# Kernel tuning notes

Measured on AMD Instinct MI355X. Metric: run time of the kernel, lower is better.

Reference implementation:

```python
import jax, jax.numpy as jnp
import numpy as np

ALPHA = 0.99   # config.alpha_grape
GAMMA = 0.999  # config.gamma
LAMBD = 0.7    # config.lambd_grape
T, A = 262144, 64


def setup_inputs() -> dict:
    key = jax.random.key(0)
    ks = jax.random.split(key, 7)
    q = jax.random.normal(ks[0], (T + 1, A), jnp.float32)
    q_tar = jax.random.normal(ks[1], (T + 1, A), jnp.float32)
    # pi / mu are probability distributions over actions (softmax of logits)
    pi = jax.nn.softmax(jax.random.normal(ks[2], (T + 1, A), jnp.float32), axis=-1)
    mu_t = jax.nn.softmax(jax.random.normal(ks[3], (T, A), jnp.float32), axis=-1)
    a_t = jax.random.randint(ks[4], (T,), 0, A, dtype=jnp.int32)
    r_t = jax.random.normal(ks[5], (T,), jnp.float32)
    done_t = jax.random.randint(ks[6], (T,), 0, 2, dtype=jnp.int32)
    return dict(q=q, q_tar=q_tar, pi=pi, a_t=a_t, r_t=r_t, mu_t=mu_t, done_t=done_t)


def reference(q, q_tar, pi, a_t, r_t, mu_t, done_t):
    # GRAPE.compute_targets
    l = q.shape[0] - 1
    idx = jnp.arange(l)
    pi_t, pi_tp1 = pi[:-1], pi[1:]
    q_t, q_tp1 = q[:-1], q_tar[1:]
    q_t_a = q_t[idx, a_t]                              # [T]
    v_t = jnp.sum(pi_t * q_t, axis=1)                  # [T]
    v_tp1 = jnp.sum(pi_tp1 * q_tp1, axis=1)            # [T]
    done_f = done_t.astype(q.dtype)
    q_t_a_est = r_t + (1.0 - done_f) * GAMMA * v_tp1
    td_error = q_t_a_est - q_t_a
    rho_t_a = pi_t[idx, a_t] / mu_t[idx, a_t]
    c_t_a = LAMBD * jnp.clip(rho_t_a, 0.0, 1.0)

    # backward-in-time first-order recurrence over y'
    def step(y_prime, xs):
        est, td, rho, c, d = xs
        y = jnp.where(d > 0.5, 0.0, y_prime)           # reset at episode end
        g = est + y
        y_new = LAMBD * GAMMA * rho * td + GAMMA * c * y
        return y_new, g

    _, g_q = jax.lax.scan(
        step, jnp.float32(0.0),
        (q_t_a_est, td_error, rho_t_a, c_t_a, done_f),
        reverse=True,
    )
    targets_q = g_q + ALPHA * (q_t_a - v_t)            # [T]
    advantages = (1.0 - ALPHA) * (q_t - v_t[:, None])  # [T, A]
    return targets_q, advantages
```

## Files before the change

### kernel.cpp

```cpp
#include <hip/hip_runtime.h>

#define GAMMA 0.999f
#define LAMBD 0.7f
#define ALPHA 0.99f

constexpr int A_DIM = 64;
constexpr int CH    = 256;
constexpr int BLK   = 256;

typedef float fx4 __attribute__((ext_vector_type(4)));

__device__ __forceinline__ float dot4(const float4& a, const float4& b) {
    return a.x*b.x + a.y*b.y + a.z*b.z + a.w*b.w;
}
__device__ __forceinline__ void nt_store4(float* p, float x, float y, float z, float w) {
    fx4 v = { x, y, z, w };
    __builtin_nontemporal_store(v, (fx4*)p);
}

__global__ __launch_bounds__(BLK, 4)
void k_main(const float* __restrict__ q, const float* __restrict__ q_tar,
            const float* __restrict__ pi, const int* __restrict__ a_t,
            const float* __restrict__ r_t, const float* __restrict__ mu_t,
            const int* __restrict__ done_t,
            float* __restrict__ adv_out, float* __restrict__ targets,
            float2* __restrict__ combL, float2* __restrict__ cab)
{
    __shared__ float sQa[CH], sPa[CH], sMa[CH], sKm[CH], sRt[CH];
    __shared__ float sV[CH], sVp[CH + 1];
    __shared__ float sCA[4], sCB[4];

    const int tid  = threadIdx.x;
    const int wave = tid >> 6, lane = tid & 63;
    const int sub  = lane >> 4, li = lane & 15;
    const int R0   = blockIdx.x * CH;

    {
        int r = R0 + tid;
        int a = a_t[r];
        sQa[tid] = q[r * A_DIM + a];
        sPa[tid] = pi[r * A_DIM + a];
        sMa[tid] = mu_t[r * A_DIM + a];
        sRt[tid] = r_t[r];
        sKm[tid] = 1.0f - (float)done_t[r];
    }
    if (tid >= 192 && tid < 208) {
        int l16 = tid - 192;
        int gE  = (R0 + CH) * A_DIM + l16 * 4;
        float4 pe = *(const float4*)&pi[gE];
        float4 qe = *(const float4*)&q_tar[gE];
        float d = dot4(pe, qe);
        #pragma unroll
        for (int off = 1; off < 16; off <<= 1) d += __shfl_xor(d, off);
        if (l16 == 0) sVp[CH] = d;
    }

    const int lrow0 = wave * 64 + sub;
    float4 piA, qA, qtA, piB, qB, qtB;
    {
        int gA = (R0 + lrow0) * A_DIM + li * 4;
        int gB = gA + 4 * A_DIM;
        piA = *(const float4*)&pi[gA];
        qA  = *(const float4*)&q[gA];
        qtA = *(const float4*)&q_tar[gA];
        piB = *(const float4*)&pi[gB];
        qB  = *(const float4*)&q[gB];
        qtB = *(const float4*)&q_tar[gB];
    }
    #pragma unroll
    for (int i = 0; i < 8; ++i) {
        float4 npiA, nqA, nqtA, npiB, nqB, nqtB;
        if (i < 7) {
            int gA = (R0 + lrow0 + (i + 1) * 8) * A_DIM + li * 4;
            int gB = gA + 4 * A_DIM;
            npiA = *(const float4*)&pi[gA];
            nqA  = *(const float4*)&q[gA];
            nqtA = *(const float4*)&q_tar[gA];
            npiB = *(const float4*)&pi[gB];
            nqB  = *(const float4*)&q[gB];
            nqtB = *(const float4*)&q_tar[gB];
        }

        int lrowA = lrow0 + i * 8;
        int lrowB = lrowA + 4;
        int gA = (R0 + lrowA) * A_DIM + li * 4;
        int gB = (R0 + lrowB) * A_DIM + li * 4;

        float d1A = dot4(piA, qA),  d2A = dot4(piA, qtA);
        float d1B = dot4(piB, qB),  d2B = dot4(piB, qtB);
        #pragma unroll
        for (int off = 1; off < 16; off <<= 1) {
            d1A += __shfl_xor(d1A, off);
            d2A += __shfl_xor(d2A, off);
            d1B += __shfl_xor(d1B, off);
            d2B += __shfl_xor(d2B, off);
        }

        nt_store4(&adv_out[gA],
                  (1.0f - ALPHA) * (qA.x - d1A), (1.0f - ALPHA) * (qA.y - d1A),
                  (1.0f - ALPHA) * (qA.z - d1A), (1.0f - ALPHA) * (qA.w - d1A));
        nt_store4(&adv_out[gB],
                  (1.0f - ALPHA) * (qB.x - d1B), (1.0f - ALPHA) * (qB.y - d1B),
                  (1.0f - ALPHA) * (qB.z - d1B), (1.0f - ALPHA) * (qB.w - d1B));

        if (li == 0) {
            sV[lrowA] = d1A;  sVp[lrowA] = d2A;
            sV[lrowB] = d1B;  sVp[lrowB] = d2B;
        }

        piA = npiA; qA = nqA; qtA = nqtA;
        piB = npiB; qB = nqB; qtB = nqtB;
    }
    __syncthreads();

    const int row = tid;
    float s0 = sV[row];
    float s1 = sVp[row + 1];
    float kmask = sKm[row];
    float qa  = sQa[row];
    float rho = sPa[row] / sMa[row];
    float est = sRt[row] + kmask * (GAMMA * s1);
    float td  = est - qa;
    float c   = LAMBD * fminf(fmaxf(rho, 0.0f), 1.0f);
    float Fa  = (LAMBD * GAMMA) * rho * td;
    float Fb  = kmask * (GAMMA * c);
    float E   = est + ALPHA * (qa - s0);

    float Ai = Fa, Bi = Fb;
    #pragma unroll
    for (int off = 1; off < 64; off <<= 1) {
        float An = __shfl_down(Ai, off);
        float Bn = __shfl_down(Bi, off);
        if (lane + off < 64) { Ai += Bi * An; Bi *= Bn; }
    }
    if (lane == 0) { sCA[wave] = Ai; sCB[wave] = Bi; }
    float Xa = __shfl_down(Ai, 1);
    float Xb = __shfl_down(Bi, 1);
    if (lane == 63) { Xa = 0.0f; Xb = 1.0f; }
    __syncthreads();

    float Ta = 0.0f, Tb = 1.0f;
    for (int s = wave + 1; s < 4; ++s) {
        Ta += Tb * sCA[s];
        Tb *= sCB[s];
    }
    Xa = Xa + Xb * Ta;
    Xb = Xb * Tb;

    float U = E + kmask * Xa;
    if (wave < 3) {
        __builtin_nontemporal_store(U, &targets[R0 + row]);
    } else {
        combL[blockIdx.x * 64 + lane] = make_float2(U, kmask * Xb);
    }
    if (tid == 0)
        cab[blockIdx.x] = make_float2(Ai + Bi * Ta, Bi * Tb);
}

__global__ __launch_bounds__(64, 8)
void k_fin(const float2* __restrict__ combL, const float2* __restrict__ cab,
           float* __restrict__ targets, int nch)
{
    const int lane = threadIdx.x, bid = blockIdx.x;

    const float4* cab4 = (const float4*)cab;
    float A = 0.0f, B = 1.0f;
    #pragma unroll
    for (int j = 0; j < 8; ++j) {
        float4 u = cab4[lane * 8 + j];
        A += B * u.x; B *= u.y;
        A += B * u.z; B *= u.w;
    }

    float Ai = A, Bi = B;
    #pragma unroll
    for (int off = 1; off < 64; off <<= 1) {
        float An = __shfl_down(Ai, off);
        float Bn = __shfl_down(Bi, off);
        if (lane + off < 64) { Ai += Bi * An; Bi *= Bn; }
    }
    float Xa = __shfl_down(Ai, 1);
    float Xb = __shfl_down(Bi, 1);
    if (lane == 63) { Xa = 0.0f; Xb = 1.0f; }

    float ye;
    int c1 = bid + 1;
    if (c1 >= nch) {
        ye = 0.0f;
    } else {
        int jq = c1 >> 4;
        float Aa = __shfl(Xa, jq);
        float Bb = __shfl(Xb, jq);
        for (int k2 = 16 * jq + 15; k2 >= c1; --k2) {
            float2 cv = cab[k2];
            Aa = cv.x + cv.y * Aa;
            Bb = cv.y * Bb;
        }
        ye = Aa;
    }

    float2 uw = combL[bid * 64 + lane];
    __builtin_nontemporal_store(uw.x + uw.y * ye,
                                &targets[bid * CH + 192 + lane]);
}

extern "C" void kernel_launch(void* const* d_in, const int* in_sizes, int n_in,
                              void* d_out, int out_size, void* d_ws, size_t ws_size,
                              hipStream_t stream) {
    const float* q      = (const float*)d_in[0];
    const float* q_tar  = (const float*)d_in[1];
    const float* pi     = (const float*)d_in[2];
    const int*   a_t    = (const int*)  d_in[3];
    const float* r_t    = (const float*)d_in[4];
    const float* mu_t   = (const float*)d_in[5];
    const int*   done_t = (const int*)  d_in[6];

    const int T   = in_sizes[3];
    const int nch = T / CH;

    float* targets = (float*)d_out;
    float* adv     = (float*)d_out + T;

    char* ws = (char*)d_ws;
    float2* combL = (float2*)ws;             ws += (size_t)8 * 64 * nch;
    float2* cab   = (float2*)ws;

    k_main<<<nch, BLK, 0, stream>>>(q, q_tar, pi, a_t, r_t, mu_t, done_t,
                                    adv, targets, combL, cab);
    k_fin<<<nch, 64, 0, stream>>>(combL, cab, targets, nch);
}
```

Measured before the change: 63.63 us.

## Replace cross-chunk scan kernel with a truncated lookahead recurrence per block

Drops the second kernel and its workspace buffers. Each block now recomputes the backward recurrence over the next 64 rows past its chunk to estimate the incoming carry, treating the carry beyond that window as zero. This works because the decay coefficient is bounded by lambda*gamma < 1 and episode resets cut the chain, so the dropped term shrinks to within float precision. In exchange, each block reads extra pi and q_tar rows from the next chunk.

New measurement: 66.81 us. 5.0% more time.

```diff
diff --git a/kernel.cpp b/kernel.cpp
--- a/kernel.cpp
+++ b/kernel.cpp
@@ -7,6 +7,7 @@
 constexpr int A_DIM = 64;
 constexpr int CH    = 256;
 constexpr int BLK   = 256;
+constexpr int OVL   = 64;
 
 typedef float fx4 __attribute__((ext_vector_type(4)));
 
@@ -24,16 +25,20 @@
             const float* __restrict__ r_t, const float* __restrict__ mu_t,
             const int* __restrict__ done_t,
             float* __restrict__ adv_out, float* __restrict__ targets,
-            float2* __restrict__ combL, float2* __restrict__ cab)
+            int nch)
 {
     __shared__ float sQa[CH], sPa[CH], sMa[CH], sKm[CH], sRt[CH];
     __shared__ float sV[CH], sVp[CH + 1];
+    __shared__ float sQa2[OVL], sRho2[OVL], sKm2[OVL], sRt2[OVL];
+    __shared__ float sVp2[OVL + 1];
     __shared__ float sCA[4], sCB[4];
+    __shared__ float sYe;
 
     const int tid  = threadIdx.x;
     const int wave = tid >> 6, lane = tid & 63;
     const int sub  = lane >> 4, li = lane & 15;
     const int R0   = blockIdx.x * CH;
+    const bool has_ovl = (blockIdx.x + 1 < nch);
 
     {
         int r = R0 + tid;
@@ -43,6 +48,14 @@
         sMa[tid] = mu_t[r * A_DIM + a];
         sRt[tid] = r_t[r];
         sKm[tid] = 1.0f - (float)done_t[r];
+    }
+    if (tid < OVL && has_ovl) {
+        int r = R0 + CH + tid;
+        int a = a_t[r];
+        sQa2[tid]  = q[r * A_DIM + a];
+        sRho2[tid] = pi[r * A_DIM + a] / mu_t[r * A_DIM + a];
+        sRt2[tid]  = r_t[r];
+        sKm2[tid]  = 1.0f - (float)done_t[r];
     }
     if (tid >= 192 && tid < 208) {
         int l16 = tid - 192;
@@ -111,6 +124,20 @@
         piA = npiA; qA = nqA; qtA = nqtA;
         piB = npiB; qB = nqB; qtB = nqtB;
     }
+
+    if (has_ovl) {
+        #pragma unroll
+        for (int i = 0; i < 2; ++i) {
+            int j = wave * 16 + i * 8 + sub;
+            int g = (R0 + CH + 1 + j) * A_DIM + li * 4;
+            float4 pe = *(const float4*)&pi[g];
+            float4 qe = *(const float4*)&q_tar[g];
+            float d = dot4(pe, qe);
+            #pragma unroll
+            for (int off = 1; off < 16; off <<= 1) d += __shfl_xor(d, off);
+            if (li == 0) sVp2[1 + j] = d;
+        }
+    }
     __syncthreads();
 
     const int row = tid;
@@ -139,69 +166,37 @@
     if (lane == 63) { Xa = 0.0f; Xb = 1.0f; }
     __syncthreads();
 
+    if (wave == 0) {
+        float Oa = 0.0f, Ob = 0.0f;
+        if (has_ovl) {
+            float km2  = sKm2[lane];
+            float qa2  = sQa2[lane];
+            float rho2 = sRho2[lane];
+            float est2 = sRt2[lane] + km2 * (GAMMA * sVp2[lane + 1]);
+            float td2  = est2 - qa2;
+            float c2   = LAMBD * fminf(fmaxf(rho2, 0.0f), 1.0f);
+            float Fa2  = (LAMBD * GAMMA) * rho2 * td2;
+            float Fb2  = km2 * (GAMMA * c2);
+            Oa = Fa2; Ob = Fb2;
+            #pragma unroll
+            for (int off = 1; off < 64; off <<= 1) {
+                float An = __shfl_down(Oa, off);
+                float Bn = __shfl_down(Ob, off);
+                if (lane + off < 64) { Oa += Ob * An; Ob *= Bn; }
+            }
+        }
+        if (lane == 0) sYe = Oa;
+    }
+    __syncthreads();
+
     float Ta = 0.0f, Tb = 1.0f;
     for (int s = wave + 1; s < 4; ++s) {
         Ta += Tb * sCA[s];
         Tb *= sCB[s];
     }
-    Xa = Xa + Xb * Ta;
-    Xb = Xb * Tb;
-
-    float U = E + kmask * Xa;
-    if (wave < 3) {
-        __builtin_nontemporal_store(U, &targets[R0 + row]);
-    } else {
-        combL[blockIdx.x * 64 + lane] = make_float2(U, kmask * Xb);
-    }
-    if (tid == 0)
-        cab[blockIdx.x] = make_float2(Ai + Bi * Ta, Bi * Tb);
-}
-
-__global__ __launch_bounds__(64, 8)
-void k_fin(const float2* __restrict__ combL, const float2* __restrict__ cab,
-           float* __restrict__ targets, int nch)
-{
-    const int lane = threadIdx.x, bid = blockIdx.x;
-
-    const float4* cab4 = (const float4*)cab;
-    float A = 0.0f, B = 1.0f;
-    #pragma unroll
-    for (int j = 0; j < 8; ++j) {
-        float4 u = cab4[lane * 8 + j];
-        A += B * u.x; B *= u.y;
-        A += B * u.z; B *= u.w;
-    }
-
-    float Ai = A, Bi = B;
-    #pragma unroll
-    for (int off = 1; off < 64; off <<= 1) {
-        float An = __shfl_down(Ai, off);
-        float Bn = __shfl_down(Bi, off);
-        if (lane + off < 64) { Ai += Bi * An; Bi *= Bn; }
-    }
-    float Xa = __shfl_down(Ai, 1);
-    float Xb = __shfl_down(Bi, 1);
-    if (lane == 63) { Xa = 0.0f; Xb = 1.0f; }
-
-    float ye;
-    int c1 = bid + 1;
-    if (c1 >= nch) {
-        ye = 0.0f;
-    } else {
-        int jq = c1 >> 4;
-        float Aa = __shfl(Xa, jq);
-        float Bb = __shfl(Xb, jq);
-        for (int k2 = 16 * jq + 15; k2 >= c1; --k2) {
-            float2 cv = cab[k2];
-            Aa = cv.x + cv.y * Aa;
-            Bb = cv.y * Bb;
-        }
-        ye = Aa;
-    }
-
-    float2 uw = combL[bid * 64 + lane];
-    __builtin_nontemporal_store(uw.x + uw.y * ye,
-                                &targets[bid * CH + 192 + lane]);
+    float ye = sYe;
+    float y_next = Xa + Xb * (Ta + Tb * ye);
+    __builtin_nontemporal_store(E + kmask * y_next, &targets[R0 + row]);
 }
 
 extern "C" void kernel_launch(void* const* d_in, const int* in_sizes, int n_in,
@@ -221,11 +216,6 @@
     float* targets = (float*)d_out;
     float* adv     = (float*)d_out + T;
 
-    char* ws = (char*)d_ws;
-    float2* combL = (float2*)ws;             ws += (size_t)8 * 64 * nch;
-    float2* cab   = (float2*)ws;
-
     k_main<<<nch, BLK, 0, stream>>>(q, q_tar, pi, a_t, r_t, mu_t, done_t,
-                                    adv, targets, combL, cab);
-    k_fin<<<nch, 64, 0, stream>>>(combL, cab, targets, nch);
-}
+                                    adv, targets, nch);
+}
```
